# Kernel optimization log

Measured on AMD Instinct MI355X. Metric: run time of the kernel, lower is better.

The kernel has to match this reference:

```python
import jax, jax.numpy as jnp
import numpy as np

H, DH, D, S, B = 8, 64, 512, 512, 2
EPS = 1e-5

def _trop_linear(x, W):
    # y[..., o] = max_i (x[..., i] + W[o, i])
    return jnp.max(x[..., None, :] + W, axis=-1)

def _layer_norm(x, gamma, beta):
    mu = jnp.mean(x, axis=-1, keepdims=True)
    var = jnp.mean((x - mu) ** 2, axis=-1, keepdims=True)
    return (x - mu) * jax.lax.rsqrt(var + EPS) * gamma + beta

def setup_inputs() -> dict:
    key = jax.random.key(0)
    ks = jax.random.split(key, 8)
    sc = lambda fan_in: 1.0 / np.sqrt(fan_in)
    return {
        "h":   jax.random.normal(ks[0], (S, B, D), jnp.float32),
        "Wq":  jax.random.normal(ks[1], (H * DH, D), jnp.float32) * sc(D),
        "Wkv": jax.random.normal(ks[2], (2 * H * DH, D), jnp.float32) * sc(D),
        "Wqt": jax.random.normal(ks[3], (DH, DH), jnp.float32),
        "Wkt": jax.random.normal(ks[4], (DH, DH), jnp.float32),
        "Wvt": jax.random.normal(ks[5], (DH, DH), jnp.float32),
        "lam": jnp.ones((1, 1, D), jnp.float32),
        "Wo":  jax.random.normal(ks[6], (D, H * DH), jnp.float32) * sc(H * DH),
        "gamma": jnp.ones((D,), jnp.float32),
        "beta":  jnp.zeros((D,), jnp.float32),
    }

def reference(h, Wq, Wkv, Wqt, Wkt, Wvt, lam, Wo, gamma, beta):
    # h: [S, B, D]; mems=None so c == h; pre_lnorm=False
    c = h
    head_q = h @ Wq.T                                # [S, B, H*DH]
    kv = c @ Wkv.T                                   # [S, B, 2*H*DH]
    head_k, head_v = jnp.split(kv, 2, axis=-1)

    norm = lambda x: jnp.log1p(jax.nn.relu(x)) - lam  # tropical normalize
    head_q, head_k, head_v = norm(head_q), norm(head_k), norm(head_v)

    # [S,B,H,DH] -> [B,S,H,DH] -> flat reshape to [B*H, S, DH] (matches torch)
    to_bh = lambda x: jnp.transpose(x.reshape(S, B, H, DH), (1, 0, 2, 3)).reshape(B * H, S, DH)
    q = _trop_linear(to_bh(head_q), Wqt)
    k = _trop_linear(to_bh(head_k), Wkt)
    v = _trop_linear(to_bh(head_v), Wvt)

    # tropical distance score: -(max_d(q-k) - min_d(q-k)) over head dim
    diff = q[:, :, None, :] - k[:, None, :, :]        # [BH, Sq, Sk, DH]
    attn_scores = -(jnp.max(diff, axis=-1) - jnp.min(diff, axis=-1))  # [BH,Sq,Sk]

    # max-plus aggregation: context = max_sk(score + v)
    sum_sv = attn_scores[..., None] + v[:, None, :, :]  # [BH, Sq, Sk, DH]
    context = jnp.max(sum_sv, axis=2)                   # [BH, Sq, DH]

    # flat reshape back (matches torch), permute, expm1
    context = context.reshape(B, H, S, DH)
    context = jnp.transpose(context, (2, 0, 1, 3))      # [S, B, H, DH]
    context = jnp.expm1(context)
    attn_vec = context.reshape(S, B, H * DH)

    attn_out = attn_vec @ Wo.T                          # [S, B, D]
    return _layer_norm(h + attn_out, gamma, beta)
```

## Files before the change

kernel.cpp:

```cpp
#include <hip/hip_runtime.h>
#include <cmath>

typedef __attribute__((ext_vector_type(8))) __bf16 bf16x8;
typedef __attribute__((ext_vector_type(4))) float f32x4;
typedef _Float16 f16;
typedef __attribute__((ext_vector_type(2))) _Float16 f16x2;

namespace {
constexpr int GP = 512;
}

__device__ inline unsigned short f2bf(float x) {
  union { float f; unsigned u; } v; v.f = x;
  unsigned r = v.u + 0x7fff + ((v.u >> 16) & 1);
  return (unsigned short)(r >> 16);
}

__device__ inline void cvt8_store(unsigned short* dst, float4 a, float4 b) {
  ushort4 lo, hi;
  lo.x = f2bf(a.x); lo.y = f2bf(a.y); lo.z = f2bf(a.z); lo.w = f2bf(a.w);
  hi.x = f2bf(b.x); hi.y = f2bf(b.y); hi.z = f2bf(b.z); hi.w = f2bf(b.w);
  *(ushort4*)dst = lo; *(ushort4*)(dst + 4) = hi;
}

__global__ __launch_bounds__(256) void k_gemm0t(const float* __restrict__ h,
    const float* __restrict__ Wq, const float* __restrict__ Wkv,
    const float* __restrict__ lam, const float* __restrict__ Wqt,
    const float* __restrict__ Wkt, const float* __restrict__ Wvt,
    f16* __restrict__ qkvh)
{
  __shared__ unsigned short As[64][72];
  __shared__ unsigned short Bs[64][72];
  __shared__ float Wl[64][65];
  __shared__ float nl[64][68];
  const int tid = threadIdx.x;
  const int bx = blockIdx.x;
  const int r0 = blockIdx.y * 64, c0 = bx * 64;
  const int which = c0 >> 9;
  const int hh = bx & 7;
  const float* Wt = (which == 0) ? Wqt : (which == 1) ? Wkt : Wvt;
  #pragma unroll
  for (int q = 0; q < 16; ++q) {
    int idx = q * 256 + tid;
    Wl[idx >> 6][idx & 63] = Wt[idx];
  }
  const int w = tid >> 6, l = tid & 63;
  const int wr = (w >> 1) * 32, wc = (w & 1) * 32;
  const int srow = tid >> 3, sk8 = (tid & 7) * 8;
  f32x4 acc[2][2] = {};
  for (int kk = 0; kk < 512; kk += 64) {
    __syncthreads();
    #pragma unroll
    for (int q2 = 0; q2 < 2; ++q2) {
      int row = srow + q2 * 32;
      const float* ap = &h[(r0 + row) * 512 + kk + sk8];
      cvt8_store(&As[row][sk8], *(const float4*)ap, *(const float4*)(ap + 4));
      int c = c0 + row;
      const float* wrp = (c < 512) ? (Wq + c * 512) : (Wkv + (c - 512) * 512);
      cvt8_store(&Bs[row][sk8], *(const float4*)&wrp[kk + sk8],
                 *(const float4*)&wrp[kk + sk8 + 4]);
    }
    __syncthreads();
    #pragma unroll
    for (int ks = 0; ks < 2; ++ks) {
      const int kc = ks * 32 + (l >> 4) * 8;
      bf16x8 a0 = *(const bf16x8*)&As[wr +      (l & 15)][kc];
      bf16x8 a1 = *(const bf16x8*)&As[wr + 16 + (l & 15)][kc];
      bf16x8 b0 = *(const bf16x8*)&Bs[wc +      (l & 15)][kc];
      bf16x8 b1 = *(const bf16x8*)&Bs[wc + 16 + (l & 15)][kc];
      acc[0][0] = __builtin_amdgcn_mfma_f32_16x16x32_bf16(a0, b0, acc[0][0], 0, 0, 0);
      acc[0][1] = __builtin_amdgcn_mfma_f32_16x16x32_bf16(a0, b1, acc[0][1], 0, 0, 0);
      acc[1][0] = __builtin_amdgcn_mfma_f32_16x16x32_bf16(a1, b0, acc[1][0], 0, 0, 0);
      acc[1][1] = __builtin_amdgcn_mfma_f32_16x16x32_bf16(a1, b1, acc[1][1], 0, 0, 0);
    }
  }
  #pragma unroll
  for (int i = 0; i < 2; ++i)
    #pragma unroll
    for (int j = 0; j < 2; ++j)
      #pragma unroll
      for (int r = 0; r < 4; ++r) {
        int rl = wr + i * 16 + (l >> 4) * 4 + r;
        int cl = wc + j * 16 + (l & 15);
        nl[rl][cl] = log1pf(fmaxf(acc[i][j][r], 0.f)) - lam[hh * 64 + cl];
      }
  __syncthreads();
  float wreg[64];
  #pragma unroll
  for (int i = 0; i < 64; ++i) wreg[i] = Wl[l][i];
  #pragma unroll 2
  for (int it = 0; it < 16; ++it) {
    int lr = w + it * 4;
    float m0 = -INFINITY, m1 = -INFINITY;
    #pragma unroll
    for (int i = 0; i < 64; i += 4) {
      f32x4 nv = *(const f32x4*)&nl[lr][i];
      float t0 = nv[0] + wreg[i],     t1 = nv[1] + wreg[i + 1];
      float t2 = nv[2] + wreg[i + 2], t3 = nv[3] + wreg[i + 3];
      m0 = fmaxf(fmaxf(m0, t0), t1);
      m1 = fmaxf(fmaxf(m1, t2), t3);
    }
    int r = r0 + lr;
    int s = r >> 1, bb = r & 1;
    int g = bb * 8 + (s >> 6);
    int p = ((s & 63) << 3) | hh;
    qkvh[which * 524288 + ((g << 9) + p) * 64 + l] = (f16)fmaxf(m0, m1);
  }
}

__global__ __launch_bounds__(256) void k_attn(const f16* __restrict__ qkv,
    f16* __restrict__ ctxp)
{
  const int pt = blockIdx.x;
  const int g  = blockIdx.y;
  const int cs = blockIdx.z;
  const f16* qb = qkv +           (size_t)g * GP * 64;
  const f16* kb = qkv + 524288  + (size_t)g * GP * 64;
  const f16* vb = qkv + 1048576 + (size_t)g * GP * 64;
  __shared__ f16 qs[64][64];
  __shared__ f16 ks[64][64];
  __shared__ f16 vs[64][64];
  __shared__ f16 ss[64][68];
  const int tid = threadIdx.x;
  const int tr = tid >> 4, tc = tid & 15;
  {
    int row = tid >> 3, blk = tid & 7;
    int c0 = cs * 64;
    #pragma unroll
    for (int q2 = 0; q2 < 2; ++q2) {
      int r = row + q2 * 32;
      int sb = (blk ^ (r & 7)) * 8;
      *(int4*)&qs[r][sb] = *(const int4*)&qb[(pt * 64 + r) * 64 + blk * 8];
      *(int4*)&ks[r][sb] = *(const int4*)&kb[(c0 + r) * 64 + blk * 8];
      *(int4*)&vs[r][sb] = *(const int4*)&vb[(c0 + r) * 64 + blk * 8];
    }
  }
  __syncthreads();
  const f16 NEGI = (f16)(-INFINITY);
  const f16 POSI = (f16)(INFINITY);
  const f16x2 NEG2 = { NEGI, NEGI };
  const f16x2 POS2 = { POSI, POSI };
  f16x2 mx2[4][4], mn2[4][4];
  #pragma unroll
  for (int i = 0; i < 4; ++i)
    #pragma unroll
    for (int m = 0; m < 4; ++m) { mx2[i][m] = NEG2; mn2[i][m] = POS2; }
  #pragma unroll
  for (int b = 0; b < 8; ++b) {
    f16x2 qv[4][4], kv[4][4];
    #pragma unroll
    for (int i = 0; i < 4; ++i) {
      int r = 4 * tr + i;
      *(int4*)&qv[i][0] = *(const int4*)&qs[r][(b ^ (r & 7)) * 8];
    }
    #pragma unroll
    for (int m = 0; m < 4; ++m)
      *(int4*)&kv[m][0] = *(const int4*)&ks[tc + 16 * m][(b ^ (tc & 7)) * 8];
    #pragma unroll
    for (int i = 0; i < 4; ++i)
      #pragma unroll
      for (int m = 0; m < 4; ++m)
        #pragma unroll
        for (int e = 0; e < 4; ++e) {
          f16x2 d = qv[i][e] - kv[m][e];
          mx2[i][m] = __builtin_elementwise_max(mx2[i][m], d);
          mn2[i][m] = __builtin_elementwise_min(mn2[i][m], d);
        }
  }
  #pragma unroll
  for (int i = 0; i < 4; ++i)
    #pragma unroll
    for (int m = 0; m < 4; ++m) {
      f16 mxv = (mx2[i][m][0] > mx2[i][m][1]) ? mx2[i][m][0] : mx2[i][m][1];
      f16 mnv = (mn2[i][m][0] < mn2[i][m][1]) ? mn2[i][m][0] : mn2[i][m][1];
      ss[tc + 16 * m][4 * tr + i] = mnv - mxv;
    }
  __syncthreads();
  f16x2 ctx[4][4];
  #pragma unroll
  for (int i = 0; i < 4; ++i)
    #pragma unroll
    for (int j = 0; j < 4; ++j) ctx[i][j] = NEG2;
  const int ch = tc >> 3, dg = tc & 7;
  #pragma unroll
  for (int gi = 0; gi < 4; ++gi) {
    #pragma unroll
    for (int e = 0; e < 8; ++e) {
      int c = ch * 32 + gi * 8 + e;
      f16x2 vv[4];
      *(int4*)&vv[0] = *(const int4*)&vs[c][(dg ^ (c & 7)) * 8];
      f16 sr[4];
      *(int2*)&sr[0] = *(const int2*)&ss[c][4 * tr];
      #pragma unroll
      for (int i = 0; i < 4; ++i) {
        f16x2 s2 = { sr[i], sr[i] };
        #pragma unroll
        for (int j = 0; j < 4; ++j)
          ctx[i][j] = __builtin_elementwise_max(ctx[i][j], s2 + vv[j]);
      }
    }
  }
  #pragma unroll
  for (int i = 0; i < 4; ++i)
    #pragma unroll
    for (int j = 0; j < 4; ++j) {
      int o = __shfl_xor(*(int*)&ctx[i][j], 8);
      ctx[i][j] = __builtin_elementwise_max(ctx[i][j], *(f16x2*)&o);
    }
  if (tc < 8) {
    size_t base = (size_t)cs * 524288 + (size_t)g * 32768
                + (size_t)(pt * 64 + 4 * tr) * 64 + dg * 8;
    #pragma unroll
    for (int i = 0; i < 4; ++i) {
      int4 o;
      ((f16x2*)&o)[0] = ctx[i][0];
      ((f16x2*)&o)[1] = ctx[i][1];
      ((f16x2*)&o)[2] = ctx[i][2];
      ((f16x2*)&o)[3] = ctx[i][3];
      *(int4*)&ctxp[base + i * 64] = o;
    }
  }
}

__global__ __launch_bounds__(256) void k_comb(const f16* __restrict__ ctxp,
    unsigned short* __restrict__ avb)
{
  int idx = blockIdx.x * 256 + threadIdx.x;
  int dblk = idx & 7, p = (idx >> 3) & 511, g = idx >> 12;
  const f16* cp = ctxp + (size_t)g * 32768 + p * 64 + dblk * 8;
  f16x2 m[4];
  *(int4*)&m[0] = *(const int4*)cp;
  #pragma unroll
  for (int cs = 1; cs < 8; ++cs) {
    f16x2 t[4];
    *(int4*)&t[0] = *(const int4*)(cp + (size_t)cs * 524288);
    #pragma unroll
    for (int e = 0; e < 4; ++e) m[e] = __builtin_elementwise_max(m[e], t[e]);
  }
  ushort4 lo, hi;
  lo.x = f2bf(expm1f((float)m[0][0]));
  lo.y = f2bf(expm1f((float)m[0][1]));
  lo.z = f2bf(expm1f((float)m[1][0]));
  lo.w = f2bf(expm1f((float)m[1][1]));
  hi.x = f2bf(expm1f((float)m[2][0]));
  hi.y = f2bf(expm1f((float)m[2][1]));
  hi.z = f2bf(expm1f((float)m[3][0]));
  hi.w = f2bf(expm1f((float)m[3][1]));
  unsigned short* dst = avb + (p * 2 + (g >> 3)) * 512 + (g & 7) * 64 + dblk * 8;
  *(ushort4*)dst = lo;
  *(ushort4*)(dst + 4) = hi;
}

__global__ __launch_bounds__(256) void k_gemm1c(const unsigned short* __restrict__ avb,
    const float* __restrict__ Wo, float* __restrict__ ao)
{
  __shared__ unsigned short As[64][72];
  __shared__ unsigned short Bs[64][72];
  const int tid = threadIdx.x;
  const int r0 = blockIdx.y * 64, c0 = blockIdx.x * 64;
  const int w = tid >> 6, l = tid & 63;
  const int wr = (w >> 1) * 32, wc = (w & 1) * 32;
  const int srow = tid >> 3, sk8 = (tid & 7) * 8;
  f32x4 acc[2][2] = {};
  for (int kk = 0; kk < 512; kk += 64) {
    __syncthreads();
    #pragma unroll
    for (int q2 = 0; q2 < 2; ++q2) {
      int row = srow + q2 * 32;
      *(int4*)&As[row][sk8] = *(const int4*)&avb[(r0 + row) * 512 + kk + sk8];
      const float* bp = &Wo[(c0 + row) * 512 + kk + sk8];
      cvt8_store(&Bs[row][sk8], *(const float4*)bp, *(const float4*)(bp + 4));
    }
    __syncthreads();
    #pragma unroll
    for (int ks = 0; ks < 2; ++ks) {
      const int kc = ks * 32 + (l >> 4) * 8;
      bf16x8 a0 = *(const bf16x8*)&As[wr +      (l & 15)][kc];
      bf16x8 a1 = *(const bf16x8*)&As[wr + 16 + (l & 15)][kc];
      bf16x8 b0 = *(const bf16x8*)&Bs[wc +      (l & 15)][kc];
      bf16x8 b1 = *(const bf16x8*)&Bs[wc + 16 + (l & 15)][kc];
      acc[0][0] = __builtin_amdgcn_mfma_f32_16x16x32_bf16(a0, b0, acc[0][0], 0, 0, 0);
      acc[0][1] = __builtin_amdgcn_mfma_f32_16x16x32_bf16(a0, b1, acc[0][1], 0, 0, 0);
      acc[1][0] = __builtin_amdgcn_mfma_f32_16x16x32_bf16(a1, b0, acc[1][0], 0, 0, 0);
      acc[1][1] = __builtin_amdgcn_mfma_f32_16x16x32_bf16(a1, b1, acc[1][1], 0, 0, 0);
    }
  }
  #pragma unroll
  for (int i = 0; i < 2; ++i)
    #pragma unroll
    for (int j = 0; j < 2; ++j)
      #pragma unroll
      for (int r = 0; r < 4; ++r) {
        int row = r0 + wr + i * 16 + (l >> 4) * 4 + r;
        int col = c0 + wc + j * 16 + (l & 15);
        ao[row * 512 + col] = acc[i][j][r];
      }
}

__global__ __launch_bounds__(256) void k_ln(const float* __restrict__ hin,
    const float* __restrict__ ao, const float* __restrict__ gamma,
    const float* __restrict__ beta, float* __restrict__ outp)
{
  const int r = blockIdx.x * 4 + (threadIdx.x >> 6);
  const int lane = threadIdx.x & 63;
  const int c0 = lane * 8;
  f32x4 h0 = *(const f32x4*)&hin[r * 512 + c0];
  f32x4 h1 = *(const f32x4*)&hin[r * 512 + c0 + 4];
  f32x4 a0 = *(const f32x4*)&ao[r * 512 + c0];
  f32x4 a1 = *(const f32x4*)&ao[r * 512 + c0 + 4];
  float x[8];
  #pragma unroll
  for (int e = 0; e < 4; ++e) { x[e] = h0[e] + a0[e]; x[4 + e] = h1[e] + a1[e]; }
  float sum = 0.f, sq = 0.f;
  #pragma unroll
  for (int e = 0; e < 8; ++e) { sum += x[e]; sq += x[e] * x[e]; }
  #pragma unroll
  for (int o = 32; o > 0; o >>= 1) {
    sum += __shfl_xor(sum, o);
    sq  += __shfl_xor(sq, o);
  }
  float mu  = sum * (1.f / 512.f);
  float var = sq * (1.f / 512.f) - mu * mu;
  float rstd = rsqrtf(fmaxf(var, 0.f) + 1e-5f);
  f32x4 o0, o1;
  #pragma unroll
  for (int e = 0; e < 4; ++e) {
    o0[e] = (x[e]     - mu) * rstd * gamma[c0 + e]     + beta[c0 + e];
    o1[e] = (x[4 + e] - mu) * rstd * gamma[c0 + 4 + e] + beta[c0 + 4 + e];
  }
  *(f32x4*)&outp[r * 512 + c0]     = o0;
  *(f32x4*)&outp[r * 512 + c0 + 4] = o1;
}

extern "C" void kernel_launch(void* const* d_in, const int* in_sizes, int n_in,
                              void* d_out, int out_size, void* d_ws, size_t ws_size,
                              hipStream_t stream) {
  const float* hin   = (const float*)d_in[0];
  const float* Wq    = (const float*)d_in[1];
  const float* Wkv   = (const float*)d_in[2];
  const float* Wqt   = (const float*)d_in[3];
  const float* Wkt   = (const float*)d_in[4];
  const float* Wvt   = (const float*)d_in[5];
  const float* lam   = (const float*)d_in[6];
  const float* Wo    = (const float*)d_in[7];
  const float* gamma = (const float*)d_in[8];
  const float* beta  = (const float*)d_in[9];
  char* wsb = (char*)d_ws;
  f16*            qkvh = (f16*)wsb;
  f16*            ctxp = (f16*)(wsb + 6291456);
  unsigned short* avb  = (unsigned short*)(wsb + 4194304);
  float*          ao   = (float*)wsb;
  float*          out  = (float*)d_out;

  k_gemm0t<<<dim3(24, 16),   256, 0, stream>>>(hin, Wq, Wkv, lam, Wqt, Wkt, Wvt, qkvh);
  k_attn  <<<dim3(8, 16, 8), 256, 0, stream>>>(qkvh, ctxp);
  k_comb  <<<dim3(256),      256, 0, stream>>>(ctxp, avb);
  k_gemm1c<<<dim3(8, 16),    256, 0, stream>>>(avb, Wo, ao);
  k_ln    <<<dim3(256),      256, 0, stream>>>(hin, ao, gamma, beta, out);
}
```

Baseline: 78.47 us.

## Fuse five kernels into one persistent megakernel with grid-wide barriers

Replaces the five separate launches (QKV GEMM plus tropical projection, attention, combine, output GEMM, layernorm) with one 1024-block kernel that separates the phases with a hierarchical atomic grid barrier, plus a small init kernel that zeroes the barrier counters. This is meant to remove per-launch overhead and inter-kernel gaps. It also moves the tropical projection weights and the normalized activations to packed f16 math in registers, and unions the shared memory of the phases. The design depends on all 1024 blocks being resident at once for the barrier to work, otherwise it can deadlock. Most blocks also sit idle in the phases that use fewer than 1024 blocks, and the reduced precision in the projection can shift the results.

```diff
diff --git a/kernel.cpp b/kernel.cpp
--- a/kernel.cpp
+++ b/kernel.cpp
@@ -5,10 +5,6 @@
 typedef __attribute__((ext_vector_type(4))) float f32x4;
 typedef _Float16 f16;
 typedef __attribute__((ext_vector_type(2))) _Float16 f16x2;
-
-namespace {
-constexpr int GP = 512;
-}
 
 __device__ inline unsigned short f2bf(float x) {
   union { float f; unsigned u; } v; v.f = x;
@@ -23,313 +19,335 @@
   *(ushort4*)dst = lo; *(ushort4*)(dst + 4) = hi;
 }
 
-__global__ __launch_bounds__(256) void k_gemm0t(const float* __restrict__ h,
-    const float* __restrict__ Wq, const float* __restrict__ Wkv,
-    const float* __restrict__ lam, const float* __restrict__ Wqt,
-    const float* __restrict__ Wkt, const float* __restrict__ Wvt,
-    f16* __restrict__ qkvh)
+struct SMemG0 { unsigned short As[64][72]; unsigned short Bs[64][72]; f16 nl[64][72]; };
+struct SMemAt { f16 qs[64][64]; f16 ks[64][64]; f16 vs[64][64]; f16 ss[64][68]; };
+union SMem { SMemG0 g0; SMemAt at; };
+
+__device__ inline void gsync(unsigned* bar) {
+  __syncthreads();
+  if (threadIdx.x == 0) {
+    __threadfence();
+    unsigned* leaf = bar + (blockIdx.x & 63) * 32;
+    unsigned* root = bar + 2048;
+    unsigned p = __hip_atomic_fetch_add(leaf, 1u, __ATOMIC_ACQ_REL,
+                                        __HIP_MEMORY_SCOPE_AGENT);
+    if (p == 15u)
+      __hip_atomic_fetch_add(root, 1u, __ATOMIC_ACQ_REL,
+                             __HIP_MEMORY_SCOPE_AGENT);
+    while (__hip_atomic_load(root, __ATOMIC_RELAXED,
+                             __HIP_MEMORY_SCOPE_AGENT) < 64u)
+      __builtin_amdgcn_s_sleep(1);
+    (void)__hip_atomic_load(root, __ATOMIC_ACQUIRE, __HIP_MEMORY_SCOPE_AGENT);
+  }
+  __syncthreads();
+}
+
+__global__ __launch_bounds__(256) void k_init(unsigned* __restrict__ bar) {
+  uint4 z; z.x = 0; z.y = 0; z.z = 0; z.w = 0;
+  *(uint4*)&bar[(blockIdx.x * 256 + threadIdx.x) * 4] = z;
+}
+
+__global__ __launch_bounds__(256, 4) void k_mega(
+    const float* __restrict__ hin, const float* __restrict__ Wq,
+    const float* __restrict__ Wkv, const float* __restrict__ lam,
+    const float* __restrict__ Wqt, const float* __restrict__ Wkt,
+    const float* __restrict__ Wvt, const float* __restrict__ Wo,
+    const float* __restrict__ gamma, const float* __restrict__ beta,
+    f16* __restrict__ qkvh, f16* __restrict__ ctxp,
+    unsigned short* __restrict__ avb, float* __restrict__ ao,
+    unsigned* __restrict__ bar, float* __restrict__ outp)
 {
-  __shared__ unsigned short As[64][72];
-  __shared__ unsigned short Bs[64][72];
-  __shared__ float Wl[64][65];
-  __shared__ float nl[64][68];
+  __shared__ SMem sm;
+  const int blk = blockIdx.x;
   const int tid = threadIdx.x;
-  const int bx = blockIdx.x;
-  const int r0 = blockIdx.y * 64, c0 = bx * 64;
-  const int which = c0 >> 9;
-  const int hh = bx & 7;
-  const float* Wt = (which == 0) ? Wqt : (which == 1) ? Wkt : Wvt;
-  #pragma unroll
-  for (int q = 0; q < 16; ++q) {
-    int idx = q * 256 + tid;
-    Wl[idx >> 6][idx & 63] = Wt[idx];
-  }
-  const int w = tid >> 6, l = tid & 63;
-  const int wr = (w >> 1) * 32, wc = (w & 1) * 32;
-  const int srow = tid >> 3, sk8 = (tid & 7) * 8;
-  f32x4 acc[2][2] = {};
-  for (int kk = 0; kk < 512; kk += 64) {
+
+  if (blk < 384) {
+    const int bx = blk % 24, by = blk / 24;
+    const int r0 = by * 64, c0 = bx * 64;
+    const int which = c0 >> 9;
+    const int hh = bx & 7;
+    const float* Wt = (which == 0) ? Wqt : (which == 1) ? Wkt : Wvt;
+    const int w = tid >> 6, l = tid & 63;
+    const int wr = (w >> 1) * 32, wc = (w & 1) * 32;
+    const int srow = tid >> 3, sk8 = (tid & 7) * 8;
+    f16x2 wreg[32];
+    #pragma unroll
+    for (int i = 0; i < 64; i += 4) {
+      f32x4 wv = *(const f32x4*)&Wt[l * 64 + i];
+      wreg[i / 2]     = f16x2{ (f16)wv[0], (f16)wv[1] };
+      wreg[i / 2 + 1] = f16x2{ (f16)wv[2], (f16)wv[3] };
+    }
+    f32x4 acc[2][2] = {};
+    for (int kk = 0; kk < 512; kk += 64) {
+      __syncthreads();
+      #pragma unroll
+      for (int q2 = 0; q2 < 2; ++q2) {
+        int row = srow + q2 * 32;
+        const float* ap = &hin[(r0 + row) * 512 + kk + sk8];
+        cvt8_store(&sm.g0.As[row][sk8], *(const float4*)ap, *(const float4*)(ap + 4));
+        int c = c0 + row;
+        const float* wrp = (c < 512) ? (Wq + c * 512) : (Wkv + (c - 512) * 512);
+        cvt8_store(&sm.g0.Bs[row][sk8], *(const float4*)&wrp[kk + sk8],
+                   *(const float4*)&wrp[kk + sk8 + 4]);
+      }
+      __syncthreads();
+      #pragma unroll
+      for (int ks = 0; ks < 2; ++ks) {
+        const int kc = ks * 32 + (l >> 4) * 8;
+        bf16x8 a0 = *(const bf16x8*)&sm.g0.As[wr +      (l & 15)][kc];
+        bf16x8 a1 = *(const bf16x8*)&sm.g0.As[wr + 16 + (l & 15)][kc];
+        bf16x8 b0 = *(const bf16x8*)&sm.g0.Bs[wc +      (l & 15)][kc];
+        bf16x8 b1 = *(const bf16x8*)&sm.g0.Bs[wc + 16 + (l & 15)][kc];
+        acc[0][0] = __builtin_amdgcn_mfma_f32_16x16x32_bf16(a0, b0, acc[0][0], 0, 0, 0);
+        acc[0][1] = __builtin_amdgcn_mfma_f32_16x16x32_bf16(a0, b1, acc[0][1], 0, 0, 0);
+        acc[1][0] = __builtin_amdgcn_mfma_f32_16x16x32_bf16(a1, b0, acc[1][0], 0, 0, 0);
+        acc[1][1] = __builtin_amdgcn_mfma_f32_16x16x32_bf16(a1, b1, acc[1][1], 0, 0, 0);
+      }
+    }
+    #pragma unroll
+    for (int i = 0; i < 2; ++i)
+      #pragma unroll
+      for (int j = 0; j < 2; ++j)
+        #pragma unroll
+        for (int r = 0; r < 4; ++r) {
+          int rl = wr + i * 16 + (l >> 4) * 4 + r;
+          int cl = wc + j * 16 + (l & 15);
+          sm.g0.nl[rl][cl] = (f16)(log1pf(fmaxf(acc[i][j][r], 0.f)) - lam[hh * 64 + cl]);
+        }
     __syncthreads();
-    #pragma unroll
-    for (int q2 = 0; q2 < 2; ++q2) {
-      int row = srow + q2 * 32;
-      const float* ap = &h[(r0 + row) * 512 + kk + sk8];
-      cvt8_store(&As[row][sk8], *(const float4*)ap, *(const float4*)(ap + 4));
-      int c = c0 + row;
-      const float* wrp = (c < 512) ? (Wq + c * 512) : (Wkv + (c - 512) * 512);
-      cvt8_store(&Bs[row][sk8], *(const float4*)&wrp[kk + sk8],
-                 *(const float4*)&wrp[kk + sk8 + 4]);
+    const f16 NEGI = (f16)(-INFINITY);
+    #pragma unroll 2
+    for (int it = 0; it < 16; ++it) {
+      int lr = w + it * 4;
+      f16x2 m2 = f16x2{ NEGI, NEGI };
+      #pragma unroll
+      for (int i = 0; i < 8; ++i) {
+        f16x2 nv[4];
+        *(int4*)&nv[0] = *(const int4*)&sm.g0.nl[lr][i * 8];
+        m2 = __builtin_elementwise_max(m2, nv[0] + wreg[i * 4 + 0]);
+        m2 = __builtin_elementwise_max(m2, nv[1] + wreg[i * 4 + 1]);
+        m2 = __builtin_elementwise_max(m2, nv[2] + wreg[i * 4 + 2]);
+        m2 = __builtin_elementwise_max(m2, nv[3] + wreg[i * 4 + 3]);
+      }
+      f16 m = (m2[0] > m2[1]) ? m2[0] : m2[1];
+      int r = r0 + lr;
+      int s = r >> 1, bb = r & 1;
+      int g = bb * 8 + (s >> 6);
+      int p = ((s & 63) << 3) | hh;
+      qkvh[which * 524288 + ((g << 9) + p) * 64 + l] = m;
+    }
+  }
+  gsync(bar);
+
+  {
+    const int pt = blk >> 7;
+    const int g  = (blk >> 3) & 15;
+    const int cs = blk & 7;
+    const f16* qb = qkvh +           (size_t)g * 512 * 64;
+    const f16* kb = qkvh + 524288  + (size_t)g * 512 * 64;
+    const f16* vb = qkvh + 1048576 + (size_t)g * 512 * 64;
+    const int tr = tid >> 4, tc = tid & 15;
+    {
+      int row = tid >> 3, blk8 = tid & 7;
+      int c0 = cs * 64;
+      #pragma unroll
+      for (int q2 = 0; q2 < 2; ++q2) {
+        int r = row + q2 * 32;
+        int sb = (blk8 ^ (r & 7)) * 8;
+        *(int4*)&sm.at.qs[r][sb] = *(const int4*)&qb[(pt * 64 + r) * 64 + blk8 * 8];
+        *(int4*)&sm.at.ks[r][sb] = *(const int4*)&kb[(c0 + r) * 64 + blk8 * 8];
+        *(int4*)&sm.at.vs[r][sb] = *(const int4*)&vb[(c0 + r) * 64 + blk8 * 8];
+      }
     }
     __syncthreads();
-    #pragma unroll
-    for (int ks = 0; ks < 2; ++ks) {
-      const int kc = ks * 32 + (l >> 4) * 8;
-      bf16x8 a0 = *(const bf16x8*)&As[wr +      (l & 15)][kc];
-      bf16x8 a1 = *(const bf16x8*)&As[wr + 16 + (l & 15)][kc];
-      bf16x8 b0 = *(const bf16x8*)&Bs[wc +      (l & 15)][kc];
-      bf16x8 b1 = *(const bf16x8*)&Bs[wc + 16 + (l & 15)][kc];
-      acc[0][0] = __builtin_amdgcn_mfma_f32_16x16x32_bf16(a0, b0, acc[0][0], 0, 0, 0);
-      acc[0][1] = __builtin_amdgcn_mfma_f32_16x16x32_bf16(a0, b1, acc[0][1], 0, 0, 0);
-      acc[1][0] = __builtin_amdgcn_mfma_f32_16x16x32_bf16(a1, b0, acc[1][0], 0, 0, 0);
-      acc[1][1] = __builtin_amdgcn_mfma_f32_16x16x32_bf16(a1, b1, acc[1][1], 0, 0, 0);
-    }
-  }
-  #pragma unroll
-  for (int i = 0; i < 2; ++i)
-    #pragma unroll
-    for (int j = 0; j < 2; ++j)
-      #pragma unroll
-      for (int r = 0; r < 4; ++r) {
-        int rl = wr + i * 16 + (l >> 4) * 4 + r;
-        int cl = wc + j * 16 + (l & 15);
-        nl[rl][cl] = log1pf(fmaxf(acc[i][j][r], 0.f)) - lam[hh * 64 + cl];
-      }
-  __syncthreads();
-  float wreg[64];
-  #pragma unroll
-  for (int i = 0; i < 64; ++i) wreg[i] = Wl[l][i];
-  #pragma unroll 2
-  for (int it = 0; it < 16; ++it) {
-    int lr = w + it * 4;
-    float m0 = -INFINITY, m1 = -INFINITY;
-    #pragma unroll
-    for (int i = 0; i < 64; i += 4) {
-      f32x4 nv = *(const f32x4*)&nl[lr][i];
-      float t0 = nv[0] + wreg[i],     t1 = nv[1] + wreg[i + 1];
-      float t2 = nv[2] + wreg[i + 2], t3 = nv[3] + wreg[i + 3];
-      m0 = fmaxf(fmaxf(m0, t0), t1);
-      m1 = fmaxf(fmaxf(m1, t2), t3);
-    }
-    int r = r0 + lr;
-    int s = r >> 1, bb = r & 1;
-    int g = bb * 8 + (s >> 6);
-    int p = ((s & 63) << 3) | hh;
-    qkvh[which * 524288 + ((g << 9) + p) * 64 + l] = (f16)fmaxf(m0, m1);
-  }
-}
-
-__global__ __launch_bounds__(256) void k_attn(const f16* __restrict__ qkv,
-    f16* __restrict__ ctxp)
-{
-  const int pt = blockIdx.x;
-  const int g  = blockIdx.y;
-  const int cs = blockIdx.z;
-  const f16* qb = qkv +           (size_t)g * GP * 64;
-  const f16* kb = qkv + 524288  + (size_t)g * GP * 64;
-  const f16* vb = qkv + 1048576 + (size_t)g * GP * 64;
-  __shared__ f16 qs[64][64];
-  __shared__ f16 ks[64][64];
-  __shared__ f16 vs[64][64];
-  __shared__ f16 ss[64][68];
-  const int tid = threadIdx.x;
-  const int tr = tid >> 4, tc = tid & 15;
-  {
-    int row = tid >> 3, blk = tid & 7;
-    int c0 = cs * 64;
-    #pragma unroll
-    for (int q2 = 0; q2 < 2; ++q2) {
-      int r = row + q2 * 32;
-      int sb = (blk ^ (r & 7)) * 8;
-      *(int4*)&qs[r][sb] = *(const int4*)&qb[(pt * 64 + r) * 64 + blk * 8];
-      *(int4*)&ks[r][sb] = *(const int4*)&kb[(c0 + r) * 64 + blk * 8];
-      *(int4*)&vs[r][sb] = *(const int4*)&vb[(c0 + r) * 64 + blk * 8];
-    }
-  }
-  __syncthreads();
-  const f16 NEGI = (f16)(-INFINITY);
-  const f16 POSI = (f16)(INFINITY);
-  const f16x2 NEG2 = { NEGI, NEGI };
-  const f16x2 POS2 = { POSI, POSI };
-  f16x2 mx2[4][4], mn2[4][4];
-  #pragma unroll
-  for (int i = 0; i < 4; ++i)
-    #pragma unroll
-    for (int m = 0; m < 4; ++m) { mx2[i][m] = NEG2; mn2[i][m] = POS2; }
-  #pragma unroll
-  for (int b = 0; b < 8; ++b) {
-    f16x2 qv[4][4], kv[4][4];
-    #pragma unroll
-    for (int i = 0; i < 4; ++i) {
-      int r = 4 * tr + i;
-      *(int4*)&qv[i][0] = *(const int4*)&qs[r][(b ^ (r & 7)) * 8];
-    }
-    #pragma unroll
-    for (int m = 0; m < 4; ++m)
-      *(int4*)&kv[m][0] = *(const int4*)&ks[tc + 16 * m][(b ^ (tc & 7)) * 8];
+    const f16 NEGI = (f16)(-INFINITY);
+    const f16 POSI = (f16)(INFINITY);
+    const f16x2 NEG2 = { NEGI, NEGI };
+    const f16x2 POS2 = { POSI, POSI };
+    f16x2 mx2[4][4], mn2[4][4];
     #pragma unroll
     for (int i = 0; i < 4; ++i)
       #pragma unroll
+      for (int m = 0; m < 4; ++m) { mx2[i][m] = NEG2; mn2[i][m] = POS2; }
+    #pragma unroll
+    for (int b = 0; b < 8; ++b) {
+      f16x2 qv[4][4], kv[4][4];
+      #pragma unroll
+      for (int i = 0; i < 4; ++i) {
+        int r = 4 * tr + i;
+        *(int4*)&qv[i][0] = *(const int4*)&sm.at.qs[r][(b ^ (r & 7)) * 8];
+      }
+      #pragma unroll
       for (int m = 0; m < 4; ++m)
+        *(int4*)&kv[m][0] = *(const int4*)&sm.at.ks[tc + 16 * m][(b ^ (tc & 7)) * 8];
+      #pragma unroll
+      for (int i = 0; i < 4; ++i)
         #pragma unroll
-        for (int e = 0; e < 4; ++e) {
-          f16x2 d = qv[i][e] - kv[m][e];
-          mx2[i][m] = __builtin_elementwise_max(mx2[i][m], d);
-          mn2[i][m] = __builtin_elementwise_min(mn2[i][m], d);
+        for (int m = 0; m < 4; ++m)
+          #pragma unroll
+          for (int e = 0; e < 4; ++e) {
+            f16x2 d = qv[i][e] - kv[m][e];
+            mx2[i][m] = __builtin_elementwise_max(mx2[i][m], d);
+            mn2[i][m] = __builtin_elementwise_min(mn2[i][m], d);
+          }
+    }
+    #pragma unroll
+    for (int i = 0; i < 4; ++i)
+      #pragma unroll
+      for (int m = 0; m < 4; ++m) {
+        f16 mxv = (mx2[i][m][0] > mx2[i][m][1]) ? mx2[i][m][0] : mx2[i][m][1];
+        f16 mnv = (mn2[i][m][0] < mn2[i][m][1]) ? mn2[i][m][0] : mn2[i][m][1];
+        sm.at.ss[tc + 16 * m][4 * tr + i] = mnv - mxv;
+      }
+    __syncthreads();
+    f16x2 ctx[4][4];
+    #pragma unroll
+    for (int i = 0; i < 4; ++i)
+      #pragma unroll
+      for (int j = 0; j < 4; ++j) ctx[i][j] = NEG2;
+    const int ch = tc >> 3, dg = tc & 7;
+    #pragma unroll
+    for (int gi = 0; gi < 4; ++gi) {
+      #pragma unroll
+      for (int e = 0; e < 8; ++e) {
+        int c = ch * 32 + gi * 8 + e;
+        f16x2 vv[4];
+        *(int4*)&vv[0] = *(const int4*)&sm.at.vs[c][(dg ^ (c & 7)) * 8];
+        f16 sr[4];
+        *(int2*)&sr[0] = *(const int2*)&sm.at.ss[c][4 * tr];
+        #pragma unroll
+        for (int i = 0; i < 4; ++i) {
+          f16x2 s2 = { sr[i], sr[i] };
+          #pragma unroll
+          for (int j = 0; j < 4; ++j)
+            ctx[i][j] = __builtin_elementwise_max(ctx[i][j], s2 + vv[j]);
         }
-  }
-  #pragma unroll
-  for (int i = 0; i < 4; ++i)
-    #pragma unroll
-    for (int m = 0; m < 4; ++m) {
-      f16 mxv = (mx2[i][m][0] > mx2[i][m][1]) ? mx2[i][m][0] : mx2[i][m][1];
-      f16 mnv = (mn2[i][m][0] < mn2[i][m][1]) ? mn2[i][m][0] : mn2[i][m][1];
-      ss[tc + 16 * m][4 * tr + i] = mnv - mxv;
-    }
-  __syncthreads();
-  f16x2 ctx[4][4];
-  #pragma unroll
-  for (int i = 0; i < 4; ++i)
-    #pragma unroll
-    for (int j = 0; j < 4; ++j) ctx[i][j] = NEG2;
-  const int ch = tc >> 3, dg = tc & 7;
-  #pragma unroll
-  for (int gi = 0; gi < 4; ++gi) {
-    #pragma unroll
-    for (int e = 0; e < 8; ++e) {
-      int c = ch * 32 + gi * 8 + e;
-      f16x2 vv[4];
-      *(int4*)&vv[0] = *(const int4*)&vs[c][(dg ^ (c & 7)) * 8];
-      f16 sr[4];
-      *(int2*)&sr[0] = *(const int2*)&ss[c][4 * tr];
+      }
+    }
+    #pragma unroll
+    for (int i = 0; i < 4; ++i)
+      #pragma unroll
+      for (int j = 0; j < 4; ++j) {
+        int o = __shfl_xor(*(int*)&ctx[i][j], 8);
+        ctx[i][j] = __builtin_elementwise_max(ctx[i][j], *(f16x2*)&o);
+      }
+    if (tc < 8) {
+      size_t base = (size_t)cs * 524288 + (size_t)g * 32768
+                  + (size_t)(pt * 64 + 4 * tr) * 64 + dg * 8;
       #pragma unroll
       for (int i = 0; i < 4; ++i) {
-        f16x2 s2 = { sr[i], sr[i] };
+        int4 o;
+        ((f16x2*)&o)[0] = ctx[i][0];
+        ((f16x2*)&o)[1] = ctx[i][1];
+        ((f16x2*)&o)[2] = ctx[i][2];
+        ((f16x2*)&o)[3] = ctx[i][3];
+        *(int4*)&ctxp[base + i * 64] = o;
+      }
+    }
+  }
+  gsync(bar + 4096);
+
+  if (blk < 256) {
+    int idx = blk * 256 + tid;
+    int dblk = idx & 7, p = (idx >> 3) & 511, g = idx >> 12;
+    const f16* cp = ctxp + (size_t)g * 32768 + p * 64 + dblk * 8;
+    f16x2 m[4];
+    *(int4*)&m[0] = *(const int4*)cp;
+    #pragma unroll
+    for (int cs = 1; cs < 8; ++cs) {
+      f16x2 t[4];
+      *(int4*)&t[0] = *(const int4*)(cp + (size_t)cs * 524288);
+      #pragma unroll
+      for (int e = 0; e < 4; ++e) m[e] = __builtin_elementwise_max(m[e], t[e]);
+    }
+    ushort4 lo, hi;
+    lo.x = f2bf(expm1f((float)m[0][0]));
+    lo.y = f2bf(expm1f((float)m[0][1]));
+    lo.z = f2bf(expm1f((float)m[1][0]));
+    lo.w = f2bf(expm1f((float)m[1][1]));
+    hi.x = f2bf(expm1f((float)m[2][0]));
+    hi.y = f2bf(expm1f((float)m[2][1]));
+    hi.z = f2bf(expm1f((float)m[3][0]));
+    hi.w = f2bf(expm1f((float)m[3][1]));
+    unsigned short* dst = avb + (p * 2 + (g >> 3)) * 512 + (g & 7) * 64 + dblk * 8;
+    *(ushort4*)dst = lo;
+    *(ushort4*)(dst + 4) = hi;
+  }
+  gsync(bar + 8192);
+
+  if (blk < 128) {
+    const int r0 = (blk >> 3) * 64, c0 = (blk & 7) * 64;
+    const int w = tid >> 6, l = tid & 63;
+    const int wr = (w >> 1) * 32, wc = (w & 1) * 32;
+    const int srow = tid >> 3, sk8 = (tid & 7) * 8;
+    f32x4 acc[2][2] = {};
+    for (int kk = 0; kk < 512; kk += 64) {
+      __syncthreads();
+      #pragma unroll
+      for (int q2 = 0; q2 < 2; ++q2) {
+        int row = srow + q2 * 32;
+        *(int4*)&sm.g0.As[row][sk8] = *(const int4*)&avb[(r0 + row) * 512 + kk + sk8];
+        const float* bp = &Wo[(c0 + row) * 512 + kk + sk8];
+        cvt8_store(&sm.g0.Bs[row][sk8], *(const float4*)bp, *(const float4*)(bp + 4));
+      }
+      __syncthreads();
+      #pragma unroll
+      for (int ks = 0; ks < 2; ++ks) {
+        const int kc = ks * 32 + (l >> 4) * 8;
+        bf16x8 a0 = *(const bf16x8*)&sm.g0.As[wr +      (l & 15)][kc];
+        bf16x8 a1 = *(const bf16x8*)&sm.g0.As[wr + 16 + (l & 15)][kc];
+        bf16x8 b0 = *(const bf16x8*)&sm.g0.Bs[wc +      (l & 15)][kc];
+        bf16x8 b1 = *(const bf16x8*)&sm.g0.Bs[wc + 16 + (l & 15)][kc];
+        acc[0][0] = __builtin_amdgcn_mfma_f32_16x16x32_bf16(a0, b0, acc[0][0], 0, 0, 0);
+        acc[0][1] = __builtin_amdgcn_mfma_f32_16x16x32_bf16(a0, b1, acc[0][1], 0, 0, 0);
+        acc[1][0] = __builtin_amdgcn_mfma_f32_16x16x32_bf16(a1, b0, acc[1][0], 0, 0, 0);
+        acc[1][1] = __builtin_amdgcn_mfma_f32_16x16x32_bf16(a1, b1, acc[1][1], 0, 0, 0);
+      }
+    }
+    #pragma unroll
+    for (int i = 0; i < 2; ++i)
+      #pragma unroll
+      for (int j = 0; j < 2; ++j)
         #pragma unroll
-        for (int j = 0; j < 4; ++j)
-          ctx[i][j] = __builtin_elementwise_max(ctx[i][j], s2 + vv[j]);
-      }
-    }
-  }
-  #pragma unroll
-  for (int i = 0; i < 4; ++i)
-    #pragma unroll
-    for (int j = 0; j < 4; ++j) {
-      int o = __shfl_xor(*(int*)&ctx[i][j], 8);
-      ctx[i][j] = __builtin_elementwise_max(ctx[i][j], *(f16x2*)&o);
-    }
-  if (tc < 8) {
-    size_t base = (size_t)cs * 524288 + (size_t)g * 32768
-                + (size_t)(pt * 64 + 4 * tr) * 64 + dg * 8;
-    #pragma unroll
-    for (int i = 0; i < 4; ++i) {
-      int4 o;
-      ((f16x2*)&o)[0] = ctx[i][0];
-      ((f16x2*)&o)[1] = ctx[i][1];
-      ((f16x2*)&o)[2] = ctx[i][2];
-      ((f16x2*)&o)[3] = ctx[i][3];
-      *(int4*)&ctxp[base + i * 64] = o;
-    }
-  }
-}
-
-__global__ __launch_bounds__(256) void k_comb(const f16* __restrict__ ctxp,
-    unsigned short* __restrict__ avb)
-{
-  int idx = blockIdx.x * 256 + threadIdx.x;
-  int dblk = idx & 7, p = (idx >> 3) & 511, g = idx >> 12;
-  const f16* cp = ctxp + (size_t)g * 32768 + p * 64 + dblk * 8;
-  f16x2 m[4];
-  *(int4*)&m[0] = *(const int4*)cp;
-  #pragma unroll
-  for (int cs = 1; cs < 8; ++cs) {
-    f16x2 t[4];
-    *(int4*)&t[0] = *(const int4*)(cp + (size_t)cs * 524288);
-    #pragma unroll
-    for (int e = 0; e < 4; ++e) m[e] = __builtin_elementwise_max(m[e], t[e]);
-  }
-  ushort4 lo, hi;
-  lo.x = f2bf(expm1f((float)m[0][0]));
-  lo.y = f2bf(expm1f((float)m[0][1]));
-  lo.z = f2bf(expm1f((float)m[1][0]));
-  lo.w = f2bf(expm1f((float)m[1][1]));
-  hi.x = f2bf(expm1f((float)m[2][0]));
-  hi.y = f2bf(expm1f((float)m[2][1]));
-  hi.z = f2bf(expm1f((float)m[3][0]));
-  hi.w = f2bf(expm1f((float)m[3][1]));
-  unsigned short* dst = avb + (p * 2 + (g >> 3)) * 512 + (g & 7) * 64 + dblk * 8;
-  *(ushort4*)dst = lo;
-  *(ushort4*)(dst + 4) = hi;
-}
-
-__global__ __launch_bounds__(256) void k_gemm1c(const unsigned short* __restrict__ avb,
-    const float* __restrict__ Wo, float* __restrict__ ao)
-{
-  __shared__ unsigned short As[64][72];
-  __shared__ unsigned short Bs[64][72];
-  const int tid = threadIdx.x;
-  const int r0 = blockIdx.y * 64, c0 = blockIdx.x * 64;
-  const int w = tid >> 6, l = tid & 63;
-  const int wr = (w >> 1) * 32, wc = (w & 1) * 32;
-  const int srow = tid >> 3, sk8 = (tid & 7) * 8;
-  f32x4 acc[2][2] = {};
-  for (int kk = 0; kk < 512; kk += 64) {
-    __syncthreads();
-    #pragma unroll
-    for (int q2 = 0; q2 < 2; ++q2) {
-      int row = srow + q2 * 32;
-      *(int4*)&As[row][sk8] = *(const int4*)&avb[(r0 + row) * 512 + kk + sk8];
-      const float* bp = &Wo[(c0 + row) * 512 + kk + sk8];
-      cvt8_store(&Bs[row][sk8], *(const float4*)bp, *(const float4*)(bp + 4));
-    }
-    __syncthreads();
-    #pragma unroll
-    for (int ks = 0; ks < 2; ++ks) {
-      const int kc = ks * 32 + (l >> 4) * 8;
-      bf16x8 a0 = *(const bf16x8*)&As[wr +      (l & 15)][kc];
-      bf16x8 a1 = *(const bf16x8*)&As[wr + 16 + (l & 15)][kc];
-      bf16x8 b0 = *(const bf16x8*)&Bs[wc +      (l & 15)][kc];
-      bf16x8 b1 = *(const bf16x8*)&Bs[wc + 16 + (l & 15)][kc];
-      acc[0][0] = __builtin_amdgcn_mfma_f32_16x16x32_bf16(a0, b0, acc[0][0], 0, 0, 0);
-      acc[0][1] = __builtin_amdgcn_mfma_f32_16x16x32_bf16(a0, b1, acc[0][1], 0, 0, 0);
-      acc[1][0] = __builtin_amdgcn_mfma_f32_16x16x32_bf16(a1, b0, acc[1][0], 0, 0, 0);
-      acc[1][1] = __builtin_amdgcn_mfma_f32_16x16x32_bf16(a1, b1, acc[1][1], 0, 0, 0);
-    }
-  }
-  #pragma unroll
-  for (int i = 0; i < 2; ++i)
-    #pragma unroll
-    for (int j = 0; j < 2; ++j)
-      #pragma unroll
-      for (int r = 0; r < 4; ++r) {
-        int row = r0 + wr + i * 16 + (l >> 4) * 4 + r;
-        int col = c0 + wc + j * 16 + (l & 15);
-        ao[row * 512 + col] = acc[i][j][r];
-      }
-}
-
-__global__ __launch_bounds__(256) void k_ln(const float* __restrict__ hin,
-    const float* __restrict__ ao, const float* __restrict__ gamma,
-    const float* __restrict__ beta, float* __restrict__ outp)
-{
-  const int r = blockIdx.x * 4 + (threadIdx.x >> 6);
-  const int lane = threadIdx.x & 63;
-  const int c0 = lane * 8;
-  f32x4 h0 = *(const f32x4*)&hin[r * 512 + c0];
-  f32x4 h1 = *(const f32x4*)&hin[r * 512 + c0 + 4];
-  f32x4 a0 = *(const f32x4*)&ao[r * 512 + c0];
-  f32x4 a1 = *(const f32x4*)&ao[r * 512 + c0 + 4];
-  float x[8];
-  #pragma unroll
-  for (int e = 0; e < 4; ++e) { x[e] = h0[e] + a0[e]; x[4 + e] = h1[e] + a1[e]; }
-  float sum = 0.f, sq = 0.f;
-  #pragma unroll
-  for (int e = 0; e < 8; ++e) { sum += x[e]; sq += x[e] * x[e]; }
-  #pragma unroll
-  for (int o = 32; o > 0; o >>= 1) {
-    sum += __shfl_xor(sum, o);
-    sq  += __shfl_xor(sq, o);
-  }
-  float mu  = sum * (1.f / 512.f);
-  float var = sq * (1.f / 512.f) - mu * mu;
-  float rstd = rsqrtf(fmaxf(var, 0.f) + 1e-5f);
-  f32x4 o0, o1;
-  #pragma unroll
-  for (int e = 0; e < 4; ++e) {
-    o0[e] = (x[e]     - mu) * rstd * gamma[c0 + e]     + beta[c0 + e];
-    o1[e] = (x[4 + e] - mu) * rstd * gamma[c0 + 4 + e] + beta[c0 + 4 + e];
-  }
-  *(f32x4*)&outp[r * 512 + c0]     = o0;
-  *(f32x4*)&outp[r * 512 + c0 + 4] = o1;
+        for (int r = 0; r < 4; ++r) {
+          int row = r0 + wr + i * 16 + (l >> 4) * 4 + r;
+          int col = c0 + wc + j * 16 + (l & 15);
+          ao[row * 512 + col] = acc[i][j][r];
+        }
+  }
+  gsync(bar + 12288);
+
+  if (blk < 256) {
+    const int r = blk * 4 + (tid >> 6);
+    const int lane = tid & 63;
+    const int c0 = lane * 8;
+    f32x4 h0 = *(const f32x4*)&hin[r * 512 + c0];
+    f32x4 h1 = *(const f32x4*)&hin[r * 512 + c0 + 4];
+    f32x4 a0 = *(const f32x4*)&ao[r * 512 + c0];
+    f32x4 a1 = *(const f32x4*)&ao[r * 512 + c0 + 4];
+    float x[8];
+    #pragma unroll
+    for (int e = 0; e < 4; ++e) { x[e] = h0[e] + a0[e]; x[4 + e] = h1[e] + a1[e]; }
+    float sum = 0.f, sq = 0.f;
+    #pragma unroll
+    for (int e = 0; e < 8; ++e) { sum += x[e]; sq += x[e] * x[e]; }
+    #pragma unroll
+    for (int o = 32; o > 0; o >>= 1) {
+      sum += __shfl_xor(sum, o);
+      sq  += __shfl_xor(sq, o);
+    }
+    float mu  = sum * (1.f / 512.f);
+    float var = sq * (1.f / 512.f) - mu * mu;
+    float rstd = rsqrtf(fmaxf(var, 0.f) + 1e-5f);
+    f32x4 o0, o1;
+    #pragma unroll
+    for (int e = 0; e < 4; ++e) {
+      o0[e] = (x[e]     - mu) * rstd * gamma[c0 + e]     + beta[c0 + e];
+      o1[e] = (x[4 + e] - mu) * rstd * gamma[c0 + 4 + e] + beta[c0 + 4 + e];
+    }
+    *(f32x4*)&outp[r * 512 + c0]     = o0;
+    *(f32x4*)&outp[r * 512 + c0 + 4] = o1;
+  }
 }
 
 extern "C" void kernel_launch(void* const* d_in, const int* in_sizes, int n_in,
@@ -347,14 +365,13 @@
   const float* beta  = (const float*)d_in[9];
   char* wsb = (char*)d_ws;
   f16*            qkvh = (f16*)wsb;
-  f16*            ctxp = (f16*)(wsb + 6291456);
-  unsigned short* avb  = (unsigned short*)(wsb + 4194304);
-  float*          ao   = (float*)wsb;
+  f16*            ctxp = (f16*)(wsb + (4u << 20));
+  unsigned short* avb  = (unsigned short*)(wsb + (13u << 20));
+  float*          ao   = (float*)(wsb + (14u << 20));
+  unsigned*       bar  = (unsigned*)(wsb + (16u << 20));
   float*          out  = (float*)d_out;
 
-  k_gemm0t<<<dim3(24, 16),   256, 0, stream>>>(hin, Wq, Wkv, lam, Wqt, Wkt, Wvt, qkvh);
-  k_attn  <<<dim3(8, 16, 8), 256, 0, stream>>>(qkvh, ctxp);
-  k_comb  <<<dim3(256),      256, 0, stream>>>(ctxp, avb);
-  k_gemm1c<<<dim3(8, 16),    256, 0, stream>>>(avb, Wo, ao);
-  k_ln    <<<dim3(256),      256, 0, stream>>>(hin, ao, gamma, beta, out);
-}
+  k_init<<<16, 256, 0, stream>>>(bar);
+  k_mega<<<1024, 256, 0, stream>>>(hin, Wq, Wkv, lam, Wqt, Wkt, Wvt, Wo,
+                                   gamma, beta, qkvh, ctxp, avb, ao, bar, out);
+}
```

Measured after the change: 282.7 us. 3.6x slower.

## Fuse combine and layernorm into producers via last-block atomic counters; f16 tropical projection

Applied to the files above, without the earlier changes.

Removes the separate combine and layernorm launches. The last split block of each attention tile now does the cross-split max and expm1, and the last column block of each GEMM row panel does residual plus layernorm. Completion is tracked with atomic tickets that the first kernel resets. The tropical per-head projection in the first GEMM also moves from fp32 to packed f16 arithmetic. Together these cut launch overhead and halve the ALU work in that stage, at the cost of serialized tail work, extra fences, and reduced precision in the max-plus projection.

```diff
diff --git a/kernel.cpp b/kernel.cpp
--- a/kernel.cpp
+++ b/kernel.cpp
@@ -27,13 +27,14 @@
     const float* __restrict__ Wq, const float* __restrict__ Wkv,
     const float* __restrict__ lam, const float* __restrict__ Wqt,
     const float* __restrict__ Wkt, const float* __restrict__ Wvt,
-    f16* __restrict__ qkvh)
+    f16* __restrict__ qkvh, unsigned* __restrict__ tick)
 {
   __shared__ unsigned short As[64][72];
   __shared__ unsigned short Bs[64][72];
   __shared__ float Wl[64][65];
-  __shared__ float nl[64][68];
+  __shared__ f16 nl[64][72];
   const int tid = threadIdx.x;
+  if (blockIdx.x == 0 && blockIdx.y == 0 && tid < 160) tick[tid] = 0u;
   const int bx = blockIdx.x;
   const int r0 = blockIdx.y * 64, c0 = bx * 64;
   const int which = c0 >> 9;
@@ -82,34 +83,39 @@
       for (int r = 0; r < 4; ++r) {
         int rl = wr + i * 16 + (l >> 4) * 4 + r;
         int cl = wc + j * 16 + (l & 15);
-        nl[rl][cl] = log1pf(fmaxf(acc[i][j][r], 0.f)) - lam[hh * 64 + cl];
-      }
-  __syncthreads();
-  float wreg[64];
-  #pragma unroll
-  for (int i = 0; i < 64; ++i) wreg[i] = Wl[l][i];
+        nl[rl][cl] = (f16)(log1pf(fmaxf(acc[i][j][r], 0.f)) - lam[hh * 64 + cl]);
+      }
+  __syncthreads();
+  f16x2 wreg[32];
+  #pragma unroll
+  for (int i = 0; i < 64; i += 2)
+    wreg[i / 2] = f16x2{ (f16)Wl[l][i], (f16)Wl[l][i + 1] };
+  const f16 NEGI = (f16)(-INFINITY);
   #pragma unroll 2
   for (int it = 0; it < 16; ++it) {
     int lr = w + it * 4;
-    float m0 = -INFINITY, m1 = -INFINITY;
-    #pragma unroll
-    for (int i = 0; i < 64; i += 4) {
-      f32x4 nv = *(const f32x4*)&nl[lr][i];
-      float t0 = nv[0] + wreg[i],     t1 = nv[1] + wreg[i + 1];
-      float t2 = nv[2] + wreg[i + 2], t3 = nv[3] + wreg[i + 3];
-      m0 = fmaxf(fmaxf(m0, t0), t1);
-      m1 = fmaxf(fmaxf(m1, t2), t3);
-    }
+    f16x2 m2 = f16x2{ NEGI, NEGI };
+    #pragma unroll
+    for (int i = 0; i < 8; ++i) {
+      f16x2 nv[4];
+      *(int4*)&nv[0] = *(const int4*)&nl[lr][i * 8];
+      m2 = __builtin_elementwise_max(m2, nv[0] + wreg[i * 4 + 0]);
+      m2 = __builtin_elementwise_max(m2, nv[1] + wreg[i * 4 + 1]);
+      m2 = __builtin_elementwise_max(m2, nv[2] + wreg[i * 4 + 2]);
+      m2 = __builtin_elementwise_max(m2, nv[3] + wreg[i * 4 + 3]);
+    }
+    f16 m = (m2[0] > m2[1]) ? m2[0] : m2[1];
     int r = r0 + lr;
     int s = r >> 1, bb = r & 1;
     int g = bb * 8 + (s >> 6);
     int p = ((s & 63) << 3) | hh;
-    qkvh[which * 524288 + ((g << 9) + p) * 64 + l] = (f16)fmaxf(m0, m1);
+    qkvh[which * 524288 + ((g << 9) + p) * 64 + l] = m;
   }
 }
 
 __global__ __launch_bounds__(256) void k_attn(const f16* __restrict__ qkv,
-    f16* __restrict__ ctxp)
+    f16* __restrict__ ctxp, unsigned short* __restrict__ avb,
+    unsigned* __restrict__ tick)
 {
   const int pt = blockIdx.x;
   const int g  = blockIdx.y;
@@ -121,18 +127,19 @@
   __shared__ f16 ks[64][64];
   __shared__ f16 vs[64][64];
   __shared__ f16 ss[64][68];
+  __shared__ unsigned lastf;
   const int tid = threadIdx.x;
   const int tr = tid >> 4, tc = tid & 15;
   {
-    int row = tid >> 3, blk = tid & 7;
+    int row = tid >> 3, blk8 = tid & 7;
     int c0 = cs * 64;
     #pragma unroll
     for (int q2 = 0; q2 < 2; ++q2) {
       int r = row + q2 * 32;
-      int sb = (blk ^ (r & 7)) * 8;
-      *(int4*)&qs[r][sb] = *(const int4*)&qb[(pt * 64 + r) * 64 + blk * 8];
-      *(int4*)&ks[r][sb] = *(const int4*)&kb[(c0 + r) * 64 + blk * 8];
-      *(int4*)&vs[r][sb] = *(const int4*)&vb[(c0 + r) * 64 + blk * 8];
+      int sb = (blk8 ^ (r & 7)) * 8;
+      *(int4*)&qs[r][sb] = *(const int4*)&qb[(pt * 64 + r) * 64 + blk8 * 8];
+      *(int4*)&ks[r][sb] = *(const int4*)&kb[(c0 + r) * 64 + blk8 * 8];
+      *(int4*)&vs[r][sb] = *(const int4*)&vb[(c0 + r) * 64 + blk8 * 8];
     }
   }
   __syncthreads();
@@ -220,42 +227,57 @@
       *(int4*)&ctxp[base + i * 64] = o;
     }
   }
-}
-
-__global__ __launch_bounds__(256) void k_comb(const f16* __restrict__ ctxp,
-    unsigned short* __restrict__ avb)
-{
-  int idx = blockIdx.x * 256 + threadIdx.x;
-  int dblk = idx & 7, p = (idx >> 3) & 511, g = idx >> 12;
-  const f16* cp = ctxp + (size_t)g * 32768 + p * 64 + dblk * 8;
-  f16x2 m[4];
-  *(int4*)&m[0] = *(const int4*)cp;
-  #pragma unroll
-  for (int cs = 1; cs < 8; ++cs) {
-    f16x2 t[4];
-    *(int4*)&t[0] = *(const int4*)(cp + (size_t)cs * 524288);
-    #pragma unroll
-    for (int e = 0; e < 4; ++e) m[e] = __builtin_elementwise_max(m[e], t[e]);
-  }
-  ushort4 lo, hi;
-  lo.x = f2bf(expm1f((float)m[0][0]));
-  lo.y = f2bf(expm1f((float)m[0][1]));
-  lo.z = f2bf(expm1f((float)m[1][0]));
-  lo.w = f2bf(expm1f((float)m[1][1]));
-  hi.x = f2bf(expm1f((float)m[2][0]));
-  hi.y = f2bf(expm1f((float)m[2][1]));
-  hi.z = f2bf(expm1f((float)m[3][0]));
-  hi.w = f2bf(expm1f((float)m[3][1]));
-  unsigned short* dst = avb + (p * 2 + (g >> 3)) * 512 + (g & 7) * 64 + dblk * 8;
-  *(ushort4*)dst = lo;
-  *(ushort4*)(dst + 4) = hi;
+  __syncthreads();
+  __threadfence();
+  if (tid == 0) {
+    unsigned t = __hip_atomic_fetch_add(&tick[g * 8 + pt], 1u,
+                                        __ATOMIC_ACQ_REL,
+                                        __HIP_MEMORY_SCOPE_AGENT);
+    lastf = (t == 7u) ? 1u : 0u;
+  }
+  __syncthreads();
+  if (lastf) {
+    __threadfence();
+    #pragma unroll
+    for (int q2 = 0; q2 < 2; ++q2) {
+      int idx = q2 * 256 + tid;
+      int dblk = idx & 7, row = idx >> 3;
+      int p = pt * 64 + row;
+      const f16* cp = ctxp + (size_t)g * 32768 + (size_t)p * 64 + dblk * 8;
+      f16x2 m[4];
+      *(int4*)&m[0] = *(const int4*)cp;
+      #pragma unroll
+      for (int cs2 = 1; cs2 < 8; ++cs2) {
+        f16x2 t4[4];
+        *(int4*)&t4[0] = *(const int4*)(cp + (size_t)cs2 * 524288);
+        #pragma unroll
+        for (int e = 0; e < 4; ++e) m[e] = __builtin_elementwise_max(m[e], t4[e]);
+      }
+      ushort4 lo, hi;
+      lo.x = f2bf(expm1f((float)m[0][0]));
+      lo.y = f2bf(expm1f((float)m[0][1]));
+      lo.z = f2bf(expm1f((float)m[1][0]));
+      lo.w = f2bf(expm1f((float)m[1][1]));
+      hi.x = f2bf(expm1f((float)m[2][0]));
+      hi.y = f2bf(expm1f((float)m[2][1]));
+      hi.z = f2bf(expm1f((float)m[3][0]));
+      hi.w = f2bf(expm1f((float)m[3][1]));
+      unsigned short* dst = avb + (p * 2 + (g >> 3)) * 512 + (g & 7) * 64 + dblk * 8;
+      *(ushort4*)dst = lo;
+      *(ushort4*)(dst + 4) = hi;
+    }
+  }
 }
 
 __global__ __launch_bounds__(256) void k_gemm1c(const unsigned short* __restrict__ avb,
-    const float* __restrict__ Wo, float* __restrict__ ao)
+    const float* __restrict__ Wo, float* __restrict__ ao,
+    const float* __restrict__ hin, const float* __restrict__ gamma,
+    const float* __restrict__ beta, float* __restrict__ outp,
+    unsigned* __restrict__ tick)
 {
   __shared__ unsigned short As[64][72];
   __shared__ unsigned short Bs[64][72];
+  __shared__ unsigned lastf;
   const int tid = threadIdx.x;
   const int r0 = blockIdx.y * 64, c0 = blockIdx.x * 64;
   const int w = tid >> 6, l = tid & 63;
@@ -295,41 +317,50 @@
         int col = c0 + wc + j * 16 + (l & 15);
         ao[row * 512 + col] = acc[i][j][r];
       }
-}
-
-__global__ __launch_bounds__(256) void k_ln(const float* __restrict__ hin,
-    const float* __restrict__ ao, const float* __restrict__ gamma,
-    const float* __restrict__ beta, float* __restrict__ outp)
-{
-  const int r = blockIdx.x * 4 + (threadIdx.x >> 6);
-  const int lane = threadIdx.x & 63;
-  const int c0 = lane * 8;
-  f32x4 h0 = *(const f32x4*)&hin[r * 512 + c0];
-  f32x4 h1 = *(const f32x4*)&hin[r * 512 + c0 + 4];
-  f32x4 a0 = *(const f32x4*)&ao[r * 512 + c0];
-  f32x4 a1 = *(const f32x4*)&ao[r * 512 + c0 + 4];
-  float x[8];
-  #pragma unroll
-  for (int e = 0; e < 4; ++e) { x[e] = h0[e] + a0[e]; x[4 + e] = h1[e] + a1[e]; }
-  float sum = 0.f, sq = 0.f;
-  #pragma unroll
-  for (int e = 0; e < 8; ++e) { sum += x[e]; sq += x[e] * x[e]; }
-  #pragma unroll
-  for (int o = 32; o > 0; o >>= 1) {
-    sum += __shfl_xor(sum, o);
-    sq  += __shfl_xor(sq, o);
-  }
-  float mu  = sum * (1.f / 512.f);
-  float var = sq * (1.f / 512.f) - mu * mu;
-  float rstd = rsqrtf(fmaxf(var, 0.f) + 1e-5f);
-  f32x4 o0, o1;
-  #pragma unroll
-  for (int e = 0; e < 4; ++e) {
-    o0[e] = (x[e]     - mu) * rstd * gamma[c0 + e]     + beta[c0 + e];
-    o1[e] = (x[4 + e] - mu) * rstd * gamma[c0 + 4 + e] + beta[c0 + 4 + e];
-  }
-  *(f32x4*)&outp[r * 512 + c0]     = o0;
-  *(f32x4*)&outp[r * 512 + c0 + 4] = o1;
+  __syncthreads();
+  __threadfence();
+  if (tid == 0) {
+    unsigned t = __hip_atomic_fetch_add(&tick[128 + blockIdx.y], 1u,
+                                        __ATOMIC_ACQ_REL,
+                                        __HIP_MEMORY_SCOPE_AGENT);
+    lastf = (t == 7u) ? 1u : 0u;
+  }
+  __syncthreads();
+  if (lastf) {
+    __threadfence();
+    const int lane = tid & 63;
+    const int cc = lane * 8;
+    #pragma unroll 2
+    for (int it = 0; it < 16; ++it) {
+      int r = r0 + it * 4 + w;
+      f32x4 h0 = *(const f32x4*)&hin[r * 512 + cc];
+      f32x4 h1 = *(const f32x4*)&hin[r * 512 + cc + 4];
+      f32x4 a0 = *(const f32x4*)&ao[r * 512 + cc];
+      f32x4 a1 = *(const f32x4*)&ao[r * 512 + cc + 4];
+      float x[8];
+      #pragma unroll
+      for (int e = 0; e < 4; ++e) { x[e] = h0[e] + a0[e]; x[4 + e] = h1[e] + a1[e]; }
+      float sum = 0.f, sq = 0.f;
+      #pragma unroll
+      for (int e = 0; e < 8; ++e) { sum += x[e]; sq += x[e] * x[e]; }
+      #pragma unroll
+      for (int o = 32; o > 0; o >>= 1) {
+        sum += __shfl_xor(sum, o);
+        sq  += __shfl_xor(sq, o);
+      }
+      float mu  = sum * (1.f / 512.f);
+      float var = sq * (1.f / 512.f) - mu * mu;
+      float rstd = rsqrtf(fmaxf(var, 0.f) + 1e-5f);
+      f32x4 o0, o1;
+      #pragma unroll
+      for (int e = 0; e < 4; ++e) {
+        o0[e] = (x[e]     - mu) * rstd * gamma[cc + e]     + beta[cc + e];
+        o1[e] = (x[4 + e] - mu) * rstd * gamma[cc + 4 + e] + beta[cc + 4 + e];
+      }
+      *(f32x4*)&outp[r * 512 + cc]     = o0;
+      *(f32x4*)&outp[r * 512 + cc + 4] = o1;
+    }
+  }
 }
 
 extern "C" void kernel_launch(void* const* d_in, const int* in_sizes, int n_in,
@@ -350,11 +381,12 @@
   f16*            ctxp = (f16*)(wsb + 6291456);
   unsigned short* avb  = (unsigned short*)(wsb + 4194304);
   float*          ao   = (float*)wsb;
+  unsigned*       tick = (unsigned*)(wsb + 15728640);
   float*          out  = (float*)d_out;
 
-  k_gemm0t<<<dim3(24, 16),   256, 0, stream>>>(hin, Wq, Wkv, lam, Wqt, Wkt, Wvt, qkvh);
-  k_attn  <<<dim3(8, 16, 8), 256, 0, stream>>>(qkvh, ctxp);
-  k_comb  <<<dim3(256),      256, 0, stream>>>(ctxp, avb);
-  k_gemm1c<<<dim3(8, 16),    256, 0, stream>>>(avb, Wo, ao);
-  k_ln    <<<dim3(256),      256, 0, stream>>>(hin, ao, gamma, beta, out);
-}
+  k_gemm0t<<<dim3(24, 16),   256, 0, stream>>>(hin, Wq, Wkv, lam, Wqt, Wkt, Wvt,
+                                               qkvh, tick);
+  k_attn  <<<dim3(8, 16, 8), 256, 0, stream>>>(qkvh, ctxp, avb, tick);
+  k_gemm1c<<<dim3(8, 16),    256, 0, stream>>>(avb, Wo, ao, hin, gamma, beta,
+                                               out, tick);
+}
```

After: 181.0 us. 2.31x slower.
